# Kernel tuning notes

Hardware: AMD Instinct MI355X
Metric: run time of the kernel (lower is better)

## Reference

```python
import jax, jax.numpy as jnp
import numpy as np

B, N, D = 8, 2048, 64  # batch, tokens, model dim (heads=1, value_dim=dim)


def _ln(x, g, b, eps=1e-5):
    m = jnp.mean(x, axis=-1, keepdims=True)
    v = jnp.var(x, axis=-1, keepdims=True)
    return (x - m) * jax.lax.rsqrt(v + eps) * g + b


def setup_inputs() -> dict:
    key = jax.random.key(0)
    ks = jax.random.split(key, 6)
    s = lambda k, shp, fan: jax.random.normal(k, shp, jnp.float32) * (fan ** -0.5)
    return {
        "x": jax.random.normal(ks[0], (B, N, D), jnp.float32),
        "Wq": s(ks[1], (D, D), D),            # to_q (no bias)
        "Wkv": s(ks[2], (D, 2 * D), D),       # to_kv -> [k | v] (no bias)
        "ln_mid_g": jnp.ones((D,), jnp.float32),
        "ln_mid_b": jnp.zeros((D,), jnp.float32),
        "rn_in_W": s(ks[3], (3 * D, D), 3 * D),  # RN inner Linear (depth 0)
        "rn_in_b": jnp.zeros((D,), jnp.float32),
        "rn_out_W": s(ks[4], (D, D), D),         # RN outer Linear (depth 0)
        "rn_out_b": jnp.zeros((D,), jnp.float32),
        "ln_out_g": jnp.ones((D,), jnp.float32),
        "ln_out_b": jnp.zeros((D,), jnp.float32),
    }


def reference(x, Wq, Wkv, ln_mid_g, ln_mid_b, rn_in_W, rn_in_b, rn_out_W, rn_out_b, ln_out_g, ln_out_b):
    d = x.shape[-1]
    # --- Relation (heads=1, context = x) ---
    q = x @ Wq                                  # [B,N,D]
    kv = x @ Wkv                                # [B,N,2D]
    k, v = kv[..., :d], kv[..., d:]
    dots = jnp.einsum('bid,bjd->bij', q, k) * (d ** -0.5)   # [B,N,N]
    w = jax.nn.softmax(dots, axis=-1)
    attn = jnp.einsum('bij,bjd->bid', w, v)                  # soft attention
    idx = jnp.argmax(w, axis=-1)                              # [B,N] hard select
    rtn = jnp.take_along_axis(v, idx[..., None], axis=1)      # gather values [B,N,D]
    rtn = attn - jax.lax.stop_gradient(attn - rtn)            # straight-through
    # --- RelationBlock tail (heads=1 => head axis is trivial) ---
    norm = _ln(rtn, ln_mid_g, ln_mid_b)                       # LN_mid per head
    pair = jnp.concatenate([norm, x, norm], axis=-1)          # [relation | residual | relation]
    mid = jax.nn.relu(pair @ rn_in_W + rn_in_b)               # RN inner (depth 0) + ReLU mid
    rn = mid @ rn_out_W + rn_out_b                            # RN outer (depth 0)
    out = _ln(rn, ln_out_g, ln_out_b) + x                     # LN_out + residual
    return out
```

## Files before the change

### kernel.cpp

```cpp
#include <hip/hip_runtime.h>
#include <float.h>

#define NB 8
#define NN 2048
#define ROWS (NB*NN)
#define JSPLIT 8
#define JRANGE (NN/JSPLIT)
#define CHUNK 64
#define NTILE (CHUNK/16)

typedef _Float16 half8 __attribute__((ext_vector_type(8)));
typedef _Float16 half4 __attribute__((ext_vector_type(4)));
typedef float f32x4 __attribute__((ext_vector_type(4)));

__global__ __launch_bounds__(256) void qkv_kernel(
    const float* __restrict__ x, const float* __restrict__ Wq,
    const float* __restrict__ Wkv,
    float* __restrict__ q, float* __restrict__ k, float* __restrict__ v) {
  __shared__ float stage[32*196];
  const int tid = threadIdx.x, lane = tid & 63, wv = tid >> 6;
  const int li = lane & 15, lg = lane >> 4;
  const size_t r0 = (size_t)blockIdx.x * 32;
  half8 xh[2][2], xl[2][2];
#pragma unroll
  for (int rt = 0; rt < 2; ++rt)
#pragma unroll
    for (int kh_ = 0; kh_ < 2; ++kh_) {
      const float* src = x + (r0 + rt*16 + li)*64 + kh_*32 + lg*8;
      float4 f0 = *(const float4*)src;
      float4 f1 = *(const float4*)(src+4);
      float vals[8] = {f0.x,f0.y,f0.z,f0.w,f1.x,f1.y,f1.z,f1.w};
#pragma unroll
      for (int e = 0; e < 8; ++e) {
        _Float16 h = (_Float16)vals[e];
        xh[rt][kh_][e] = h;
        xl[rt][kh_][e] = (_Float16)((vals[e] - (float)h) * 2048.0f);
      }
    }
  half8 wh[3][2], wl[3][2];
#pragma unroll
  for (int ci = 0; ci < 3; ++ci) {
    const int ct = wv*3 + ci;
    const int c  = ct*16 + li;
    const float* base; int strideW;
    if (ct < 4) { base = Wq + c; strideW = 64; }
    else        { base = Wkv + (c - 64); strideW = 128; }
#pragma unroll
    for (int kh_ = 0; kh_ < 2; ++kh_) {
      const int kbase = kh_*32 + lg*8;
#pragma unroll
      for (int e = 0; e < 8; ++e) {
        float val = base[(size_t)(kbase + e) * strideW];
        _Float16 h = (_Float16)val;
        wh[ci][kh_][e] = h;
        wl[ci][kh_][e] = (_Float16)((val - (float)h) * 2048.0f);
      }
    }
  }
  const f32x4 Z = {0.f,0.f,0.f,0.f};
#pragma unroll
  for (int rt = 0; rt < 2; ++rt)
#pragma unroll
    for (int ci = 0; ci < 3; ++ci) {
      f32x4 hh = __builtin_amdgcn_mfma_f32_16x16x32_f16(wh[ci][0], xh[rt][0], Z, 0,0,0);
      hh = __builtin_amdgcn_mfma_f32_16x16x32_f16(wh[ci][1], xh[rt][1], hh, 0,0,0);
      f32x4 xx = __builtin_amdgcn_mfma_f32_16x16x32_f16(wl[ci][0], xh[rt][0], Z, 0,0,0);
      xx = __builtin_amdgcn_mfma_f32_16x16x32_f16(wl[ci][1], xh[rt][1], xx, 0,0,0);
      xx = __builtin_amdgcn_mfma_f32_16x16x32_f16(wh[ci][0], xl[rt][0], xx, 0,0,0);
      xx = __builtin_amdgcn_mfma_f32_16x16x32_f16(wh[ci][1], xl[rt][1], xx, 0,0,0);
      const float c2 = 1.0f/2048.0f;
      float s0 = fmaf(xx[0], c2, hh[0]);
      float s1 = fmaf(xx[1], c2, hh[1]);
      float s2 = fmaf(xx[2], c2, hh[2]);
      float s3 = fmaf(xx[3], c2, hh[3]);
      *(float4*)&stage[(rt*16 + li)*196 + (wv*3+ci)*16 + lg*4] = make_float4(s0,s1,s2,s3);
    }
  __syncthreads();
  const size_t obase = r0 * 64;
#pragma unroll
  for (int it = 0; it < 2; ++it) {
    const int off = it*1024 + tid*4;
    const int row = off >> 6, col = off & 63;
    *(float4*)(q + obase + off) = *(const float4*)&stage[row*196 + col];
    *(float4*)(k + obase + off) = *(const float4*)&stage[row*196 + 64 + col];
    *(float4*)(v + obase + off) = *(const float4*)&stage[row*196 + 128 + col];
  }
}

__global__ __launch_bounds__(256,4) void argmax_mfma_kernel(
    const float* __restrict__ q, const float* __restrict__ k,
    float* __restrict__ pm, int* __restrict__ pt) {
  __shared__ _Float16 kls[2][8][CHUNK][8];
  const int tid = threadIdx.x, lane = tid & 63, wv = tid >> 6;
  const int id = blockIdx.x;
  const int b  = id & 7;
  const int ib = (id >> 3) & 15;
  const int js = id >> 7;
  const int i0 = ib*128 + wv*32;
  const int lg = lane >> 4, li = lane & 15;
  half8 qh[2][2], ql[2][2];
#pragma unroll
  for (int c = 0; c < 2; ++c)
#pragma unroll
    for (int w = 0; w < 2; ++w) {
      const float* src = q + ((size_t)(b*NN + i0 + c*16 + li))*64 + w*32 + lg*8;
      float4 f0 = *(const float4*)src;
      float4 f1 = *(const float4*)(src+4);
      float vals[8] = {f0.x,f0.y,f0.z,f0.w,f1.x,f1.y,f1.z,f1.w};
#pragma unroll
      for (int e = 0; e < 8; ++e) {
        _Float16 h = (_Float16)vals[e];
        qh[c][w][e] = h;
        ql[c][w][e] = (_Float16)((vals[e] - (float)h) * 2048.0f);
      }
    }
  const f32x4 Z = {0.f,0.f,0.f,0.f};
  float mrun[2] = {-FLT_MAX, -FLT_MAX};
  int   trun[2] = {0, 0};
  const int j0base = js*JRANGE;
#pragma unroll 1
  for (int ch = 0; ch < JRANGE/CHUNK; ++ch) {
    const int j0 = j0base + ch*CHUNK;
    __syncthreads();
#pragma unroll
    for (int it = 0; it < 4; ++it) {
      int c = it*256 + tid;
      int j = c & 63, dq = c >> 6;
      const float4 f = *(const float4*)(k + ((size_t)(b*NN + j0 + j))*64 + dq*4);
      float vv[4] = {f.x,f.y,f.z,f.w};
      half4 h, l;
#pragma unroll
      for (int e = 0; e < 4; ++e) {
        _Float16 hh = (_Float16)vv[e];
        h[e] = hh;
        l[e] = (_Float16)((vv[e] - (float)hh) * 2048.0f);
      }
      int d0 = dq >> 1, eo = (dq & 1)*4;
      *(half4*)&kls[0][d0][j][eo] = h;
      *(half4*)&kls[1][d0][j][eo] = l;
    }
    __syncthreads();
#pragma unroll
    for (int jt = 0; jt < NTILE; ++jt) {
      half8 akh0 = *(const half8*)&kls[0][lg  ][jt*16+li][0];
      half8 akh1 = *(const half8*)&kls[0][4+lg][jt*16+li][0];
      half8 akl0 = *(const half8*)&kls[1][lg  ][jt*16+li][0];
      half8 akl1 = *(const half8*)&kls[1][4+lg][jt*16+li][0];
      const int gtile = j0/16 + jt;
#pragma unroll
      for (int c = 0; c < 2; ++c) {
        f32x4 hh = __builtin_amdgcn_mfma_f32_16x16x32_f16(akh0, qh[c][0], Z, 0,0,0);
        hh = __builtin_amdgcn_mfma_f32_16x16x32_f16(akh1, qh[c][1], hh, 0,0,0);
        f32x4 xx = __builtin_amdgcn_mfma_f32_16x16x32_f16(akl0, qh[c][0], Z, 0,0,0);
        xx = __builtin_amdgcn_mfma_f32_16x16x32_f16(akl1, qh[c][1], xx, 0,0,0);
        xx = __builtin_amdgcn_mfma_f32_16x16x32_f16(akh0, ql[c][0], xx, 0,0,0);
        xx = __builtin_amdgcn_mfma_f32_16x16x32_f16(akh1, ql[c][1], xx, 0,0,0);
        const float c2 = 1.0f/2048.0f;
        float s0 = fmaf(xx[0], c2, hh[0]);
        float s1 = fmaf(xx[1], c2, hh[1]);
        float s2 = fmaf(xx[2], c2, hh[2]);
        float s3 = fmaf(xx[3], c2, hh[3]);
        float tmax = fmaxf(fmaxf(s0,s1), fmaxf(s2,s3));
        if (tmax > mrun[c]) { mrun[c] = tmax; trun[c] = gtile; }
      }
    }
  }
#pragma unroll
  for (int c = 0; c < 2; ++c) {
#pragma unroll
    for (int mask = 16; mask <= 32; mask <<= 1) {
      float om = __shfl_xor(mrun[c], mask, 64);
      int   ot = __shfl_xor(trun[c], mask, 64);
      if (om > mrun[c] || (om == mrun[c] && ot < trun[c])) { mrun[c]=om; trun[c]=ot; }
    }
  }
  if (lane < 16) {
    size_t r = (size_t)js*ROWS + b*NN + i0 + lane;
    pm[r] = mrun[0]; pt[r] = trun[0];
  } else if (lane < 32) {
    size_t r = (size_t)js*ROWS + b*NN + i0 + 16 + (lane & 15);
    pm[r] = mrun[1]; pt[r] = trun[1];
  }
}

__global__ __launch_bounds__(256) void epilogue_kernel(
    const float* __restrict__ x, const float* __restrict__ v,
    const float* __restrict__ q, const float* __restrict__ k,
    const float* __restrict__ pm, const int* __restrict__ pt,
    const float* __restrict__ g1, const float* __restrict__ b1,
    const float* __restrict__ W1, const float* __restrict__ bin,
    const float* __restrict__ W2, const float* __restrict__ bout,
    const float* __restrict__ g2, const float* __restrict__ b2,
    float* __restrict__ out) {
  __shared__ float mids[16*68];
  __shared__ float2 sums[16*4];
  __shared__ int sidx[32];
  const int tid = threadIdx.x, lane = tid & 63, wv = tid >> 6;
  const int li = lane & 15, lg = lane >> 4;
  const int bid = blockIdx.x;
  const size_t r0 = (size_t)(bid & 7)*NN + (size_t)(bid >> 3)*32;

#pragma unroll
  for (int rnd = 0; rnd < 2; ++rnd) {
    const int rloc = rnd*16 + wv*4 + lg;
    const int row  = (int)r0 + rloc;
    const int b    = row >> 11;
    float m = -FLT_MAX; int t = 0x7fffffff;
    if (li < 8) { m = pm[(size_t)li*ROWS + row]; t = pt[(size_t)li*ROWS + row]; }
#pragma unroll
    for (int mask = 1; mask <= 8; mask <<= 1) {
      float om = __shfl_xor(m, mask, 64);
      int   ot = __shfl_xor(t, mask, 64);
      if (om > m || (om == m && ot < t)) { m = om; t = ot; }
    }
    const int j = t*16 + li;
    const float4* qp = (const float4*)(q + (size_t)row*64);
    const float4* kp = (const float4*)(k + ((size_t)(b*NN) + j)*64);
    float a0=0.f,a1=0.f,a2=0.f,a3=0.f;
#pragma unroll
    for (int d4 = 0; d4 < 16; ++d4) {
      float4 qv = qp[d4], kv = kp[d4];
      a0 = fmaf(qv.x,kv.x,a0); a1 = fmaf(qv.y,kv.y,a1);
      a2 = fmaf(qv.z,kv.z,a2); a3 = fmaf(qv.w,kv.w,a3);
    }
    float dot = (a0+a1)+(a2+a3);
    int bj = j;
#pragma unroll
    for (int mask = 1; mask <= 8; mask <<= 1) {
      float od = __shfl_xor(dot, mask, 64);
      int   oj = __shfl_xor(bj, mask, 64);
      if (od > dot || (od == dot && oj < bj)) { dot = od; bj = oj; }
    }
    if (li == 0) sidx[rloc] = bj;
  }

  half8 wah[2], wal[2], wbh[2], wbl[2], w2h[2], w2l[2];
  const int ocol = wv*16 + li;
#pragma unroll
  for (int kh_ = 0; kh_ < 2; ++kh_) {
#pragma unroll
    for (int e = 0; e < 8; ++e) {
      const int d = kh_*32 + lg*8 + e;
      float wa = W1[d*64 + ocol] + W1[(128+d)*64 + ocol];
      float wb = W1[(64+d)*64 + ocol];
      float w2 = W2[d*64 + ocol];
      _Float16 h;
      h = (_Float16)wa; wah[kh_][e]=h; wal[kh_][e]=(_Float16)((wa-(float)h)*2048.f);
      h = (_Float16)wb; wbh[kh_][e]=h; wbl[kh_][e]=(_Float16)((wb-(float)h)*2048.f);
      h = (_Float16)w2; w2h[kh_][e]=h; w2l[kh_][e]=(_Float16)((w2-(float)h)*2048.f);
    }
  }
  float ga[16], bb[16];
  *(float4*)&ga[0]  = *(const float4*)(g1 + lg*8);
  *(float4*)&ga[4]  = *(const float4*)(g1 + lg*8 + 4);
  *(float4*)&ga[8]  = *(const float4*)(g1 + 32 + lg*8);
  *(float4*)&ga[12] = *(const float4*)(g1 + 32 + lg*8 + 4);
  *(float4*)&bb[0]  = *(const float4*)(b1 + lg*8);
  *(float4*)&bb[4]  = *(const float4*)(b1 + lg*8 + 4);
  *(float4*)&bb[8]  = *(const float4*)(b1 + 32 + lg*8);
  *(float4*)&bb[12] = *(const float4*)(b1 + 32 + lg*8 + 4);
  const float4 binv  = *(const float4*)(bin + wv*16 + lg*4);
  const float4 boutv = *(const float4*)(bout + wv*16 + lg*4);
  const float4 g2v   = *(const float4*)(g2 + wv*16 + lg*4);
  const float4 b2v   = *(const float4*)(b2 + wv*16 + lg*4);
  __syncthreads();

  const f32x4 Z = {0.f,0.f,0.f,0.f};
  const float c2 = 1.0f/2048.0f;
#pragma unroll 1
  for (int p = 0; p < 2; ++p) {
    const int rr = (int)r0 + p*16 + li;
    const int b  = rr >> 11;
    const int j  = sidx[p*16 + li];
    const float* vsrc = v + ((size_t)b*NN + j)*64 + lg*8;
    const float* xsrc = x + (size_t)rr*64 + lg*8;
    float vv[16], xv[16];
    *(float4*)&vv[0]  = *(const float4*)(vsrc);
    *(float4*)&vv[4]  = *(const float4*)(vsrc+4);
    *(float4*)&vv[8]  = *(const float4*)(vsrc+32);
    *(float4*)&vv[12] = *(const float4*)(vsrc+36);
    *(float4*)&xv[0]  = *(const float4*)(xsrc);
    *(float4*)&xv[4]  = *(const float4*)(xsrc+4);
    *(float4*)&xv[8]  = *(const float4*)(xsrc+32);
    *(float4*)&xv[12] = *(const float4*)(xsrc+36);
    float s = 0.f, s2 = 0.f;
#pragma unroll
    for (int e = 0; e < 16; ++e) { s += vv[e]; s2 += vv[e]*vv[e]; }
#pragma unroll
    for (int mask = 16; mask <= 32; mask <<= 1) {
      s  += __shfl_xor(s,  mask, 64);
      s2 += __shfl_xor(s2, mask, 64);
    }
    float mu  = s*(1.f/64.f);
    float inv = rsqrtf(s2*(1.f/64.f) - mu*mu + 1e-5f);
    half8 nh[2], nl[2], xh[2], xl[2];
#pragma unroll
    for (int kh_ = 0; kh_ < 2; ++kh_)
#pragma unroll
      for (int e = 0; e < 8; ++e) {
        float nvv = (vv[kh_*8+e] - mu)*inv*ga[kh_*8+e] + bb[kh_*8+e];
        _Float16 h = (_Float16)nvv;
        nh[kh_][e] = h; nl[kh_][e] = (_Float16)((nvv - (float)h)*2048.f);
        float xvv = xv[kh_*8+e];
        h = (_Float16)xvv;
        xh[kh_][e] = h; xl[kh_][e] = (_Float16)((xvv - (float)h)*2048.f);
      }
    f32x4 hh = __builtin_amdgcn_mfma_f32_16x16x32_f16(wah[0], nh[0], Z, 0,0,0);
    hh = __builtin_amdgcn_mfma_f32_16x16x32_f16(wah[1], nh[1], hh, 0,0,0);
    hh = __builtin_amdgcn_mfma_f32_16x16x32_f16(wbh[0], xh[0], hh, 0,0,0);
    hh = __builtin_amdgcn_mfma_f32_16x16x32_f16(wbh[1], xh[1], hh, 0,0,0);
    f32x4 xx = __builtin_amdgcn_mfma_f32_16x16x32_f16(wal[0], nh[0], Z, 0,0,0);
    xx = __builtin_amdgcn_mfma_f32_16x16x32_f16(wal[1], nh[1], xx, 0,0,0);
    xx = __builtin_amdgcn_mfma_f32_16x16x32_f16(wah[0], nl[0], xx, 0,0,0);
    xx = __builtin_amdgcn_mfma_f32_16x16x32_f16(wah[1], nl[1], xx, 0,0,0);
    xx = __builtin_amdgcn_mfma_f32_16x16x32_f16(wbl[0], xh[0], xx, 0,0,0);
    xx = __builtin_amdgcn_mfma_f32_16x16x32_f16(wbl[1], xh[1], xx, 0,0,0);
    xx = __builtin_amdgcn_mfma_f32_16x16x32_f16(wbh[0], xl[0], xx, 0,0,0);
    xx = __builtin_amdgcn_mfma_f32_16x16x32_f16(wbh[1], xl[1], xx, 0,0,0);
    float mv0 = fmaxf(fmaf(xx[0], c2, hh[0]) + binv.x, 0.f);
    float mv1 = fmaxf(fmaf(xx[1], c2, hh[1]) + binv.y, 0.f);
    float mv2 = fmaxf(fmaf(xx[2], c2, hh[2]) + binv.z, 0.f);
    float mv3 = fmaxf(fmaf(xx[3], c2, hh[3]) + binv.w, 0.f);
    *(float4*)&mids[li*68 + wv*16 + lg*4] = make_float4(mv0,mv1,mv2,mv3);
    __syncthreads();
    half8 mh[2], ml[2];
#pragma unroll
    for (int kh_ = 0; kh_ < 2; ++kh_) {
      float mm[8];
      *(float4*)&mm[0] = *(const float4*)&mids[li*68 + kh_*32 + lg*8];
      *(float4*)&mm[4] = *(const float4*)&mids[li*68 + kh_*32 + lg*8 + 4];
#pragma unroll
      for (int e = 0; e < 8; ++e) {
        _Float16 h = (_Float16)mm[e];
        mh[kh_][e] = h; ml[kh_][e] = (_Float16)((mm[e] - (float)h)*2048.f);
      }
    }
    __syncthreads();
    f32x4 h2 = __builtin_amdgcn_mfma_f32_16x16x32_f16(w2h[0], mh[0], Z, 0,0,0);
    h2 = __builtin_amdgcn_mfma_f32_16x16x32_f16(w2h[1], mh[1], h2, 0,0,0);
    f32x4 x2 = __builtin_amdgcn_mfma_f32_16x16x32_f16(w2l[0], mh[0], Z, 0,0,0);
    x2 = __builtin_amdgcn_mfma_f32_16x16x32_f16(w2l[1], mh[1], x2, 0,0,0);
    x2 = __builtin_amdgcn_mfma_f32_16x16x32_f16(w2h[0], ml[0], x2, 0,0,0);
    x2 = __builtin_amdgcn_mfma_f32_16x16x32_f16(w2h[1], ml[1], x2, 0,0,0);
    float rn[4];
    rn[0] = fmaf(x2[0], c2, h2[0]) + boutv.x;
    rn[1] = fmaf(x2[1], c2, h2[1]) + boutv.y;
    rn[2] = fmaf(x2[2], c2, h2[2]) + boutv.z;
    rn[3] = fmaf(x2[3], c2, h2[3]) + boutv.w;
    float ps = rn[0]+rn[1]+rn[2]+rn[3];
    float ps2 = rn[0]*rn[0]+rn[1]*rn[1]+rn[2]*rn[2]+rn[3]*rn[3];
#pragma unroll
    for (int mask = 16; mask <= 32; mask <<= 1) {
      ps  += __shfl_xor(ps,  mask, 64);
      ps2 += __shfl_xor(ps2, mask, 64);
    }
    if (lg == 0) sums[li*4 + wv] = make_float2(ps, ps2);
    __syncthreads();
    float ts = 0.f, ts2 = 0.f;
#pragma unroll
    for (int w = 0; w < 4; ++w) { float2 pp = sums[li*4 + w]; ts += pp.x; ts2 += pp.y; }
    float mu2  = ts*(1.f/64.f);
    float inv2 = rsqrtf(ts2*(1.f/64.f) - mu2*mu2 + 1e-5f);
    float4 xnv = *(const float4*)(x + (size_t)rr*64 + wv*16 + lg*4);
    float4 ov;
    ov.x = (rn[0]-mu2)*inv2*g2v.x + b2v.x + xnv.x;
    ov.y = (rn[1]-mu2)*inv2*g2v.y + b2v.y + xnv.y;
    ov.z = (rn[2]-mu2)*inv2*g2v.z + b2v.z + xnv.z;
    ov.w = (rn[3]-mu2)*inv2*g2v.w + b2v.w + xnv.w;
    *(float4*)&mids[li*68 + wv*16 + lg*4] = ov;
    __syncthreads();
    const int row = tid >> 4, col = (tid & 15)*4;
    *(float4*)(out + (r0 + p*16)*64 + tid*4) = *(const float4*)&mids[row*68 + col];
    __syncthreads();
  }
}

extern "C" void kernel_launch(void* const* d_in, const int* in_sizes, int n_in,
                              void* d_out, int out_size, void* d_ws, size_t ws_size,
                              hipStream_t stream) {
  const float* x    = (const float*)d_in[0];
  const float* Wq   = (const float*)d_in[1];
  const float* Wkv  = (const float*)d_in[2];
  const float* g1   = (const float*)d_in[3];
  const float* b1   = (const float*)d_in[4];
  const float* W1   = (const float*)d_in[5];
  const float* bin  = (const float*)d_in[6];
  const float* W2   = (const float*)d_in[7];
  const float* bout = (const float*)d_in[8];
  const float* g2   = (const float*)d_in[9];
  const float* b2   = (const float*)d_in[10];
  float* ws   = (float*)d_ws;
  float* q    = ws;
  float* k    = ws + 1048576;
  float* v    = ws + 2097152;
  float* pm   = ws + 3145728;
  int*   pt   = (int*)(ws + 3276800);

  qkv_kernel<<<ROWS/32, 256, 0, stream>>>(x, Wq, Wkv, q, k, v);
  argmax_mfma_kernel<<<16*JSPLIT*NB, 256, 0, stream>>>(q, k, pm, pt);
  epilogue_kernel<<<ROWS/32, 256, 0, stream>>>(x, v, q, k, pm, pt, g1, b1, W1, bin,
                                               W2, bout, g2, b2, (float*)d_out);
}
```

Measured before the change: 52.73 us.

## Double-buffer K chunks in argmax kernel with register prefetch and padded LDS

The argmax kernel now prefetches the next K chunk into registers while MFMAs run on the current LDS buffer, then converts it to fp16 hi/lo and writes it into the alternate buffer. This leaves one __syncthreads per chunk instead of two. The LDS row dimension is padded from 64 to 66 to reduce bank conflicts, and the global load pattern changes so each thread reads contiguous row segments. The cost is double the LDS footprint and more live registers, which could lower occupancy under the 4-blocks launch bound.

```diff
diff --git a/kernel.cpp b/kernel.cpp
--- a/kernel.cpp
+++ b/kernel.cpp
@@ -8,6 +8,7 @@
 #define JRANGE (NN/JSPLIT)
 #define CHUNK 64
 #define NTILE (CHUNK/16)
+#define NCHUNK (JRANGE/CHUNK)
 
 typedef _Float16 half8 __attribute__((ext_vector_type(8)));
 typedef _Float16 half4 __attribute__((ext_vector_type(4)));
@@ -87,10 +88,30 @@
   }
 }
 
+#define WRITEBUF(BUF)                                                     \
+  {                                                                       \
+    _Pragma("unroll")                                                     \
+    for (int it = 0; it < 4; ++it) {                                      \
+      const int j = it*16 + (tid >> 4);                                   \
+      const int dq = tid & 15;                                            \
+      float vv4[4] = {fst[it].x, fst[it].y, fst[it].z, fst[it].w};        \
+      half4 h, l;                                                         \
+      _Pragma("unroll")                                                   \
+      for (int e = 0; e < 4; ++e) {                                       \
+        _Float16 hh_ = (_Float16)vv4[e];                                  \
+        h[e] = hh_;                                                       \
+        l[e] = (_Float16)((vv4[e] - (float)hh_) * 2048.0f);               \
+      }                                                                   \
+      const int d0 = dq >> 1, eo = (dq & 1)*4;                            \
+      *(half4*)&kls[BUF][0][d0][j][eo] = h;                               \
+      *(half4*)&kls[BUF][1][d0][j][eo] = l;                               \
+    }                                                                     \
+  }
+
 __global__ __launch_bounds__(256,4) void argmax_mfma_kernel(
     const float* __restrict__ q, const float* __restrict__ k,
     float* __restrict__ pm, int* __restrict__ pt) {
-  __shared__ _Float16 kls[2][8][CHUNK][8];
+  __shared__ _Float16 kls[2][2][8][66][8];
   const int tid = threadIdx.x, lane = tid & 63, wv = tid >> 6;
   const int id = blockIdx.x;
   const int b  = id & 7;
@@ -118,34 +139,29 @@
   float mrun[2] = {-FLT_MAX, -FLT_MAX};
   int   trun[2] = {0, 0};
   const int j0base = js*JRANGE;
+  const int srow = tid >> 4, sdq = tid & 15;
+  float4 fst[4];
+#pragma unroll
+  for (int it = 0; it < 4; ++it)
+    fst[it] = *(const float4*)(k + ((size_t)(b*NN + j0base + it*16 + srow))*64 + sdq*4);
+  WRITEBUF(0);
 #pragma unroll 1
-  for (int ch = 0; ch < JRANGE/CHUNK; ++ch) {
+  for (int ch = 0; ch < NCHUNK; ++ch) {
+    __syncthreads();
+    if (ch + 1 < NCHUNK) {
+      const int j0n = j0base + (ch+1)*CHUNK;
+#pragma unroll
+      for (int it = 0; it < 4; ++it)
+        fst[it] = *(const float4*)(k + ((size_t)(b*NN + j0n + it*16 + srow))*64 + sdq*4);
+    }
+    const int buf = ch & 1;
     const int j0 = j0base + ch*CHUNK;
-    __syncthreads();
-#pragma unroll
-    for (int it = 0; it < 4; ++it) {
-      int c = it*256 + tid;
-      int j = c & 63, dq = c >> 6;
-      const float4 f = *(const float4*)(k + ((size_t)(b*NN + j0 + j))*64 + dq*4);
-      float vv[4] = {f.x,f.y,f.z,f.w};
-      half4 h, l;
-#pragma unroll
-      for (int e = 0; e < 4; ++e) {
-        _Float16 hh = (_Float16)vv[e];
-        h[e] = hh;
-        l[e] = (_Float16)((vv[e] - (float)hh) * 2048.0f);
-      }
-      int d0 = dq >> 1, eo = (dq & 1)*4;
-      *(half4*)&kls[0][d0][j][eo] = h;
-      *(half4*)&kls[1][d0][j][eo] = l;
-    }
-    __syncthreads();
 #pragma unroll
     for (int jt = 0; jt < NTILE; ++jt) {
-      half8 akh0 = *(const half8*)&kls[0][lg  ][jt*16+li][0];
-      half8 akh1 = *(const half8*)&kls[0][4+lg][jt*16+li][0];
-      half8 akl0 = *(const half8*)&kls[1][lg  ][jt*16+li][0];
-      half8 akl1 = *(const half8*)&kls[1][4+lg][jt*16+li][0];
+      half8 akh0 = *(const half8*)&kls[buf][0][lg  ][jt*16+li][0];
+      half8 akh1 = *(const half8*)&kls[buf][0][4+lg][jt*16+li][0];
+      half8 akl0 = *(const half8*)&kls[buf][1][lg  ][jt*16+li][0];
+      half8 akl1 = *(const half8*)&kls[buf][1][4+lg][jt*16+li][0];
       const int gtile = j0/16 + jt;
 #pragma unroll
       for (int c = 0; c < 2; ++c) {
@@ -164,6 +180,7 @@
         if (tmax > mrun[c]) { mrun[c] = tmax; trun[c] = gtile; }
       }
     }
+    if (ch + 1 < NCHUNK) WRITEBUF((ch+1)&1);
   }
 #pragma unroll
   for (int c = 0; c < 2; ++c) {
```

New measurement: 56.07 us. +6.3%, slower.
